# Kernel tuning notes

Measured on AMD Instinct MI355X. Metric: run time of the kernel, lower is better.

## Reference

```python
import jax, jax.numpy as jnp
import numpy as np

E, H, I, T = 8, 1024, 4096, 8192  # experts, hidden, intermediate, total tokens


def setup_inputs() -> dict:
    key = jax.random.key(0)
    k1, k2, k3 = jax.random.split(key, 3)
    hiddens = jax.random.normal(k1, (T, H), dtype=jnp.float32)
    # expert weights, scaled like standard init
    w1_weight = jax.random.normal(k2, (E, H, I), dtype=jnp.float32) * (1.0 / np.sqrt(H).astype(np.float32))
    w2_weight = jax.random.normal(k3, (E, I, H), dtype=jnp.float32) * (1.0 / np.sqrt(I).astype(np.float32))
    # tokens are pre-grouped by expert; equal load of T//E tokens per expert
    batch_sizes = jnp.full((E,), T // E, dtype=jnp.int32)
    return {"hiddens": hiddens, "batch_sizes": batch_sizes,
            "w1_weight": w1_weight, "w2_weight": w2_weight}


def _gmm(x, w, batch_sizes):
    """Grouped matmul: rows of x are grouped contiguously by expert.
    x: [T, K], w: [E, K, N], batch_sizes: [E] (sums to T). Returns [T, N].
    Loop is over the small fixed expert count; each iteration is a dense
    GEMM with rows outside the expert's segment masked to zero.
    """
    n_experts = w.shape[0]
    ends = jnp.cumsum(batch_sizes)
    starts = ends - batch_sizes
    tok = jnp.arange(x.shape[0])[:, None]  # [T, 1]
    out = jnp.zeros((x.shape[0], w.shape[2]), dtype=x.dtype)
    for e in range(n_experts):
        mask = (tok >= starts[e]) & (tok < ends[e])  # [T, 1]
        out = out + jnp.where(mask, x, jnp.zeros((), x.dtype)) @ w[e]
    return out


def reference(hiddens, batch_sizes, w1_weight, w2_weight):
    up = _gmm(hiddens, w1_weight, batch_sizes)    # [T, I]
    down = _gmm(up, w2_weight, batch_sizes)       # [T, H]
    return down
```

## Files before the change

kernel.cpp:

```cpp
#include <hip/hip_runtime.h>
#include <hip/hip_bf16.h>


typedef unsigned short u16;
typedef unsigned int u32;
typedef __attribute__((ext_vector_type(8))) short bf16x8;
typedef __attribute__((ext_vector_type(4))) float f32x4;
typedef __attribute__((ext_vector_type(4))) u32 u32x4;

#define E_N 8
#define H_N 1024
#define I_N 4096
#define T_N 8192

#define GLD2LDS16(g, l)                                                        \
  __builtin_amdgcn_global_load_lds(                                            \
      (const __attribute__((address_space(1))) void*)(g),                      \
      (__attribute__((address_space(3))) void*)(l), 16, 0, 0)

__device__ __forceinline__ u32 pkbf(float lo, float hi) {
  u32 a = __float_as_uint(lo) + 0x8000u;
  u32 b = __float_as_uint(hi) + 0x8000u;
  return __builtin_amdgcn_perm(b, a, 0x07060302u);
}

__device__ __forceinline__ u16 f2bf(float f) {
  __hip_bfloat16 h = __float2bfloat16(f);
  return *(reinterpret_cast<u16*>(&h));
}

__device__ __forceinline__ f32x4 ntload4(const float* p) {
  return __builtin_nontemporal_load((const f32x4*)p);
}

__device__ __forceinline__ int xcd_swz(int bid, int nwg) {
  const int chunk = nwg >> 3;
  return (bid & 7) * chunk + (bid >> 3);
}

#define NB_W1 16384
#define NB_X 4096
#define NB_TR 8192

__global__ __launch_bounds__(256) void prepass_kernel(
    const float* __restrict__ w1, const float* __restrict__ x,
    const float* __restrict__ w2, u16* __restrict__ w1b,
    u16* __restrict__ xb, u16* __restrict__ w2t) {
  __shared__ float tile[64 * 65];
  const int tid = threadIdx.x;
  const int bid = blockIdx.x;

  if (bid < NB_W1 + NB_X) {
    const float* src;
    u16* dst;
    size_t base;
    if (bid < NB_W1) {
      src = w1; dst = w1b; base = (size_t)bid * 2048;
    } else {
      src = x; dst = xb; base = (size_t)(bid - NB_W1) * 2048;
    }
    const size_t i = base + (size_t)tid * 8;
    f32x4 a = ntload4(src + i);
    f32x4 b = ntload4(src + i + 4);
    *(u32x4*)(dst + i) = (u32x4){pkbf(a.x, a.y), pkbf(a.z, a.w),
                                 pkbf(b.x, b.y), pkbf(b.z, b.w)};
    return;
  }

  const int b = bid - (NB_W1 + NB_X);
  const int e = b >> 10;
  const int rem = b & 1023;
  const int i0 = (rem >> 4) * 64;
  const int h0 = (rem & 15) * 64;
  const float* src = w2 + (size_t)e * I_N * H_N;
  u16* dst = w2t + (size_t)e * H_N * I_N;

  {
    const int r = tid >> 4;
    const int c4 = (tid & 15) * 4;
#pragma unroll
    for (int rr = 0; rr < 4; rr++) {
      const int row = rr * 16 + r;
      f32x4 v = ntload4(src + (size_t)(i0 + row) * H_N + h0 + c4);
      tile[row * 65 + c4 + 0] = v.x;
      tile[row * 65 + c4 + 1] = v.y;
      tile[row * 65 + c4 + 2] = v.z;
      tile[row * 65 + c4 + 3] = v.w;
    }
  }
  __syncthreads();

  {
    const int hr = tid >> 3;
    const int ic = (tid & 7) * 8;
#pragma unroll
    for (int hh = 0; hh < 2; hh++) {
      const int h = hh * 32 + hr;
      u32 p[4];
#pragma unroll
      for (int j = 0; j < 4; j++)
        p[j] = pkbf(tile[(ic + 2 * j) * 65 + h], tile[(ic + 2 * j + 1) * 65 + h]);
      *(u32x4*)(dst + (size_t)(h0 + h) * I_N + i0 + ic) =
          (u32x4){p[0], p[1], p[2], p[3]};
    }
  }
}

__global__ __launch_bounds__(256) void wgemm_kernel(const u16* __restrict__ w2t,
                                                    const u16* __restrict__ w1b,
                                                    u16* __restrict__ mt) {
  __shared__ u16 ldsA[4096];
  __shared__ u16 ldsB[4096];

  const int tid = threadIdx.x;
  const int lane = tid & 63;
  const int wv = tid >> 6;
  const int wm = wv >> 1, wn = wv & 1;
  const int lm = lane & 15, quad = lane >> 4;

  const int sbid = xcd_swz(blockIdx.x, 512);
  const int e = sbid >> 6;
  const int t = sbid & 63;
  const int row0 = (t >> 3) * 128;
  const int col0 = (t & 7) * 128;

  const u16* Ae = w2t + (size_t)e * H_N * I_N;
  const u16* Be = w1b + (size_t)e * H_N * I_N;
  u16* mte = mt + (size_t)e * H_N * H_N;

  const int s_r = tid >> 2;
  const int s_k = (tid & 3) * 8;
  const u16* gA0 = Ae + (size_t)(row0 + s_r) * I_N + s_k;
  const u16* gA1 = gA0 + (size_t)64 * I_N;
  const u16* gB0 = Be + (size_t)(col0 + s_r) * I_N + s_k;
  const u16* gB1 = gB0 + (size_t)64 * I_N;
  u16* ldsA_dst = ldsA + wv * 512;
  u16* ldsB_dst = ldsB + wv * 512;

  f32x4 acc[4][4];
#pragma unroll
  for (int i = 0; i < 4; i++)
#pragma unroll
    for (int j = 0; j < 4; j++) acc[i][j] = (f32x4){0.f, 0.f, 0.f, 0.f};

  for (int k0 = 0; k0 < I_N; k0 += 32) {
    GLD2LDS16(gA0 + k0, ldsA_dst);
    GLD2LDS16(gA1 + k0, ldsA_dst + 2048);
    GLD2LDS16(gB0 + k0, ldsB_dst);
    GLD2LDS16(gB1 + k0, ldsB_dst + 2048);

    __syncthreads();

    bf16x8 af[4], bfr[4];
#pragma unroll
    for (int mi = 0; mi < 4; mi++)
      af[mi] = *(const bf16x8*)(ldsA + (wm * 64 + mi * 16 + lm) * 32 + quad * 8);
#pragma unroll
    for (int ni = 0; ni < 4; ni++)
      bfr[ni] = *(const bf16x8*)(ldsB + (wn * 64 + ni * 16 + lm) * 32 + quad * 8);
#pragma unroll
    for (int mi = 0; mi < 4; mi++)
#pragma unroll
      for (int ni = 0; ni < 4; ni++)
        acc[mi][ni] = __builtin_amdgcn_mfma_f32_16x16x32_bf16(
            af[mi], bfr[ni], acc[mi][ni], 0, 0, 0);

    __syncthreads();
  }

  const int orow = row0 + wm * 64 + quad * 4;
  const int ocol = col0 + wn * 64 + lm;
#pragma unroll
  for (int mi = 0; mi < 4; mi++)
#pragma unroll
    for (int ni = 0; ni < 4; ni++)
#pragma unroll
      for (int r = 0; r < 4; r++)
        mte[(size_t)(orow + mi * 16 + r) * H_N + ocol + ni * 16] =
            f2bf(acc[mi][ni][r]);
}

__global__ __launch_bounds__(512, 2) void wgemm8_kernel(
    const u16* __restrict__ w2t, const u16* __restrict__ w1b,
    float* __restrict__ mtp) {
  __shared__ u16 lds[65536];

  const int tid = threadIdx.x;
  const int lane = tid & 63;
  const int wv = tid >> 6;
  const int wm = wv >> 2;
  const int wn = wv & 3;
  const int lm = lane & 15, quad = lane >> 4;

  const int sbid = xcd_swz(blockIdx.x, 256);
  const int kh = sbid >> 7;
  const int rem = sbid & 127;
  const int e = rem >> 4;
  const int t = rem & 15;
  const int row0 = (t >> 2) * 256;
  const int col0 = (t & 3) * 256;

  const u16* Ae = w2t + (size_t)e * H_N * I_N;
  const u16* Be = w1b + (size_t)e * H_N * I_N;

  const int srow = tid >> 3;
  const int koff = ((tid & 7) ^ (srow & 7)) * 8;
  const u16* gA = Ae + (size_t)(row0 + srow) * I_N + koff;
  const u16* gB = Be + (size_t)(col0 + srow) * I_N + koff;
  u16* stA = lds + wv * 512;
  u16* stB = stA + 16384;

  const int sw = (lm & 7) << 4;
  const int c0 = (((quad << 4)) ^ sw) >> 1;
  const int c1 = ((64 | (quad << 4)) ^ sw) >> 1;
  const int rdA = (wm * 128 + lm) * 64;
  const int rdB = (wn * 64 + lm) * 64;

  f32x4 acc[8][4];
#pragma unroll
  for (int i = 0; i < 8; i++)
#pragma unroll
    for (int j = 0; j < 4; j++) acc[i][j] = (f32x4){0.f, 0.f, 0.f, 0.f};

  const int kbeg = kh * (I_N / 2);
  const int NT = (I_N / 2) / 64;

#define STAGE8(bsel, k0)                                                       \
  do {                                                                         \
    u16* la = stA + (bsel)*32768;                                              \
    u16* lb = stB + (bsel)*32768;                                              \
    const u16* ga = gA + (k0);                                                 \
    const u16* gb = gB + (k0);                                                 \
    GLD2LDS16(ga, la);                                                         \
    GLD2LDS16(ga + (size_t)64 * I_N, la + 4096);                               \
    GLD2LDS16(ga + (size_t)128 * I_N, la + 8192);                              \
    GLD2LDS16(ga + (size_t)192 * I_N, la + 12288);                             \
    GLD2LDS16(gb, lb);                                                         \
    GLD2LDS16(gb + (size_t)64 * I_N, lb + 4096);                               \
    GLD2LDS16(gb + (size_t)128 * I_N, lb + 8192);                              \
    GLD2LDS16(gb + (size_t)192 * I_N, lb + 12288);                             \
  } while (0)

  STAGE8(0, kbeg);
  for (int kt = 0; kt < NT; ++kt) {
    if (kt + 1 < NT) {
      STAGE8((kt + 1) & 1, kbeg + (kt + 1) * 64);
      asm volatile("s_waitcnt vmcnt(8)" ::: "memory");
    } else {
      asm volatile("s_waitcnt vmcnt(0)" ::: "memory");
    }
    asm volatile("s_barrier" ::: "memory");

    const u16* bufA = lds + (kt & 1) * 32768;
    const u16* bufB = bufA + 16384;
#pragma unroll
    for (int kh2 = 0; kh2 < 2; ++kh2) {
      const int cc = kh2 ? c1 : c0;
      bf16x8 a[8], b[4];
#pragma unroll
      for (int ni = 0; ni < 4; ni++)
        b[ni] = *(const bf16x8*)(bufB + rdB + ni * 1024 + cc);
#pragma unroll
      for (int mi = 0; mi < 8; mi++)
        a[mi] = *(const bf16x8*)(bufA + rdA + mi * 1024 + cc);
      __builtin_amdgcn_s_setprio(1);
#pragma unroll
      for (int mi = 0; mi < 8; mi++)
#pragma unroll
        for (int ni = 0; ni < 4; ni++)
          acc[mi][ni] = __builtin_amdgcn_mfma_f32_16x16x32_bf16(
              a[mi], b[ni], acc[mi][ni], 0, 0, 0);
      __builtin_amdgcn_s_setprio(0);
    }
    asm volatile("s_barrier" ::: "memory");
  }
#undef STAGE8

  float* dst = mtp + (size_t)(kh * E_N + e) * H_N * H_N;
  const int orow = row0 + wm * 128 + quad * 4;
  const int ocol = col0 + wn * 64 + lm;
#pragma unroll
  for (int mi = 0; mi < 8; mi++)
#pragma unroll
    for (int ni = 0; ni < 4; ni++)
#pragma unroll
      for (int r = 0; r < 4; r++)
        __builtin_nontemporal_store(
            acc[mi][ni][r],
            dst + (size_t)(orow + mi * 16 + r) * H_N + ocol + ni * 16);
}

template <int KSPLIT>
__global__ __launch_bounds__(256) void reduce_mt_kernel(
    const float* __restrict__ mtp, u16* __restrict__ mt) {
  const size_t i = ((size_t)blockIdx.x * 256 + threadIdx.x) * 8;
  float s[8];
#pragma unroll
  for (int j = 0; j < 8; j++) s[j] = 0.f;
#pragma unroll
  for (int p = 0; p < KSPLIT; p++) {
    const float* q = mtp + (size_t)p * E_N * H_N * H_N + i;
    f32x4 a = ntload4(q);
    f32x4 b = ntload4(q + 4);
    s[0] += a.x; s[1] += a.y; s[2] += a.z; s[3] += a.w;
    s[4] += b.x; s[5] += b.y; s[6] += b.z; s[7] += b.w;
  }
  *(u32x4*)(mt + i) = (u32x4){pkbf(s[0], s[1]), pkbf(s[2], s[3]),
                              pkbf(s[4], s[5]), pkbf(s[6], s[7])};
}

__global__ __launch_bounds__(256) void tgemm_kernel(const u16* __restrict__ xb,
                                                    const int* __restrict__ bsz,
                                                    const u16* __restrict__ mt,
                                                    float* __restrict__ out) {
  __shared__ u16 ldsA[2048];
  __shared__ u16 ldsB[4096];

  const int tid = threadIdx.x;
  const int lane = tid & 63;
  const int wv = tid >> 6;
  const int wm = wv >> 1, wn = wv & 1;
  const int lm = lane & 15, quad = lane >> 4;

  const int sbid = xcd_swz(blockIdx.x, 1024);
  const int bm = sbid >> 3, bn = sbid & 7;
  const int row0 = bm * 64;
  const int col0 = bn * 128;

  int e = 0, start = 0;
#pragma unroll
  for (int i = 0; i < E_N; i++) {
    int b = bsz[i];
    if (row0 >= start + b) { start += b; e = i + 1; }
  }
  const u16* mte = mt + (size_t)e * H_N * H_N;

  const int s_r = tid >> 2;
  const int s_k = (tid & 3) * 8;
  const u16* gA0 = xb + (size_t)(row0 + s_r) * H_N + s_k;
  const u16* gB0 = mte + (size_t)(col0 + s_r) * H_N + s_k;
  const u16* gB1 = gB0 + (size_t)64 * H_N;
  u16* ldsA_dst = ldsA + wv * 512;
  u16* ldsB_dst = ldsB + wv * 512;

  f32x4 acc[2][4];
#pragma unroll
  for (int i = 0; i < 2; i++)
#pragma unroll
    for (int j = 0; j < 4; j++) acc[i][j] = (f32x4){0.f, 0.f, 0.f, 0.f};

  for (int k0 = 0; k0 < H_N; k0 += 32) {
    GLD2LDS16(gA0 + k0, ldsA_dst);
    GLD2LDS16(gB0 + k0, ldsB_dst);
    GLD2LDS16(gB1 + k0, ldsB_dst + 2048);

    __syncthreads();

    bf16x8 af[2], bfr[4];
#pragma unroll
    for (int mi = 0; mi < 2; mi++)
      af[mi] = *(const bf16x8*)(ldsA + (wm * 32 + mi * 16 + lm) * 32 + quad * 8);
#pragma unroll
    for (int ni = 0; ni < 4; ni++)
      bfr[ni] = *(const bf16x8*)(ldsB + (wn * 64 + ni * 16 + lm) * 32 + quad * 8);
#pragma unroll
    for (int mi = 0; mi < 2; mi++)
#pragma unroll
      for (int ni = 0; ni < 4; ni++)
        acc[mi][ni] = __builtin_amdgcn_mfma_f32_16x16x32_bf16(
            af[mi], bfr[ni], acc[mi][ni], 0, 0, 0);

    __syncthreads();
  }

  const int orow = row0 + wm * 32 + quad * 4;
  const int ocol = col0 + wn * 64 + lm;
#pragma unroll
  for (int mi = 0; mi < 2; mi++)
#pragma unroll
    for (int ni = 0; ni < 4; ni++)
#pragma unroll
      for (int r = 0; r < 4; r++)
        __builtin_nontemporal_store(
            acc[mi][ni][r],
            out + (size_t)(orow + mi * 16 + r) * H_N + ocol + ni * 16);
}

extern "C" void kernel_launch(void* const* d_in, const int* in_sizes, int n_in,
                              void* d_out, int out_size, void* d_ws,
                              size_t ws_size, hipStream_t stream) {
  (void)in_sizes; (void)n_in; (void)out_size;
  const float* hiddens = (const float*)d_in[0];
  const int* bsz = (const int*)d_in[1];
  const float* w1 = (const float*)d_in[2];
  const float* w2 = (const float*)d_in[3];
  float* out = (float*)d_out;

  char* ws = (char*)d_ws;
  u16* w1b = (u16*)(ws);
  u16* w2t = (u16*)(ws + (size_t)64 * 1024 * 1024);
  u16* xb  = (u16*)(ws + (size_t)128 * 1024 * 1024);
  u16* mt  = (u16*)(ws + (size_t)144 * 1024 * 1024);
  float* mtp = (float*)(ws + (size_t)160 * 1024 * 1024);
  const size_t MiB = 1024 * 1024;

  prepass_kernel<<<dim3(NB_W1 + NB_X + NB_TR), 256, 0, stream>>>(
      w1, hiddens, w2, w1b, xb, w2t);

  if (ws_size >= 224 * MiB) {
    wgemm8_kernel<<<dim3(256), 512, 0, stream>>>(w2t, w1b, mtp);
    reduce_mt_kernel<2><<<dim3(4096), 256, 0, stream>>>(mtp, mt);
  } else {
    wgemm_kernel<<<dim3(512), 256, 0, stream>>>(w2t, w1b, mt);
  }

  tgemm_kernel<<<dim3(1024), 256, 0, stream>>>(xb, bsz, mt, out);
}
```

Before: 410.1 us.

## Rewrite token GEMM with larger tiles, double-buffered LDS and swizzled loads

Replaces the final token-by-fused-weight GEMM with a 512-thread kernel that computes 128x256 tiles, moving from 1024 blocks to 256. K-steps grow to 64 and the LDS stages are double-buffered, so the next tile's loads overlap the current MFMAs. LDS rows use an XOR swizzle to cut bank conflicts, and MFMA issue priority is raised. The larger tile gives more reuse per load, but at 256 blocks occupancy and load balance across CUs may suffer.

```diff
diff --git a/kernel.cpp b/kernel.cpp
--- a/kernel.cpp
+++ b/kernel.cpp
@@ -309,23 +309,23 @@
                               pkbf(s[4], s[5]), pkbf(s[6], s[7])};
 }
 
-__global__ __launch_bounds__(256) void tgemm_kernel(const u16* __restrict__ xb,
-                                                    const int* __restrict__ bsz,
-                                                    const u16* __restrict__ mt,
-                                                    float* __restrict__ out) {
-  __shared__ u16 ldsA[2048];
-  __shared__ u16 ldsB[4096];
+__global__ __launch_bounds__(512, 2) void tgemm8_kernel(
+    const u16* __restrict__ xb, const int* __restrict__ bsz,
+    const u16* __restrict__ mt, float* __restrict__ out) {
+  __shared__ u16 lds[49152];
 
   const int tid = threadIdx.x;
   const int lane = tid & 63;
   const int wv = tid >> 6;
-  const int wm = wv >> 1, wn = wv & 1;
+  const int wm = wv >> 2;
+  const int wn = wv & 3;
   const int lm = lane & 15, quad = lane >> 4;
 
-  const int sbid = xcd_swz(blockIdx.x, 1024);
-  const int bm = sbid >> 3, bn = sbid & 7;
-  const int row0 = bm * 64;
-  const int col0 = bn * 128;
+  const int sbid = xcd_swz(blockIdx.x, 256);
+  const int bm = sbid >> 2;
+  const int bn = sbid & 3;
+  const int row0 = bm * 128;
+  const int col0 = bn * 256;
 
   int e = 0, start = 0;
 #pragma unroll
@@ -335,48 +335,80 @@
   }
   const u16* mte = mt + (size_t)e * H_N * H_N;
 
-  const int s_r = tid >> 2;
-  const int s_k = (tid & 3) * 8;
-  const u16* gA0 = xb + (size_t)(row0 + s_r) * H_N + s_k;
-  const u16* gB0 = mte + (size_t)(col0 + s_r) * H_N + s_k;
-  const u16* gB1 = gB0 + (size_t)64 * H_N;
-  u16* ldsA_dst = ldsA + wv * 512;
-  u16* ldsB_dst = ldsB + wv * 512;
-
-  f32x4 acc[2][4];
-#pragma unroll
-  for (int i = 0; i < 2; i++)
+  const int srow = tid >> 3;
+  const int koff = ((tid & 7) ^ (srow & 7)) * 8;
+  const u16* gA = xb + (size_t)(row0 + srow) * H_N + koff;
+  const u16* gB = mte + (size_t)(col0 + srow) * H_N + koff;
+  u16* stA = lds + wv * 512;
+  u16* stB = stA + 8192;
+
+  const int sw = (lm & 7) << 4;
+  const int c0 = (((quad << 4)) ^ sw) >> 1;
+  const int c1 = ((64 | (quad << 4)) ^ sw) >> 1;
+  const int rdA = (wm * 64 + lm) * 64;
+  const int rdB = (wn * 64 + lm) * 64;
+
+  f32x4 acc[4][4];
+#pragma unroll
+  for (int i = 0; i < 4; i++)
 #pragma unroll
     for (int j = 0; j < 4; j++) acc[i][j] = (f32x4){0.f, 0.f, 0.f, 0.f};
 
-  for (int k0 = 0; k0 < H_N; k0 += 32) {
-    GLD2LDS16(gA0 + k0, ldsA_dst);
-    GLD2LDS16(gB0 + k0, ldsB_dst);
-    GLD2LDS16(gB1 + k0, ldsB_dst + 2048);
-
-    __syncthreads();
-
-    bf16x8 af[2], bfr[4];
-#pragma unroll
-    for (int mi = 0; mi < 2; mi++)
-      af[mi] = *(const bf16x8*)(ldsA + (wm * 32 + mi * 16 + lm) * 32 + quad * 8);
-#pragma unroll
-    for (int ni = 0; ni < 4; ni++)
-      bfr[ni] = *(const bf16x8*)(ldsB + (wn * 64 + ni * 16 + lm) * 32 + quad * 8);
-#pragma unroll
-    for (int mi = 0; mi < 2; mi++)
+  const int NT = H_N / 64;
+
+#define TSTAGE6(bsel, k0)                                                      \
+  do {                                                                         \
+    u16* la = stA + (bsel)*24576;                                              \
+    u16* lb = stB + (bsel)*24576;                                              \
+    const u16* ga = gA + (k0);                                                 \
+    const u16* gb = gB + (k0);                                                 \
+    GLD2LDS16(ga, la);                                                         \
+    GLD2LDS16(ga + (size_t)64 * H_N, la + 4096);                               \
+    GLD2LDS16(gb, lb);                                                         \
+    GLD2LDS16(gb + (size_t)64 * H_N, lb + 4096);                               \
+    GLD2LDS16(gb + (size_t)128 * H_N, lb + 8192);                              \
+    GLD2LDS16(gb + (size_t)192 * H_N, lb + 12288);                             \
+  } while (0)
+
+  TSTAGE6(0, 0);
+  for (int kt = 0; kt < NT; ++kt) {
+    if (kt + 1 < NT) {
+      TSTAGE6((kt + 1) & 1, (kt + 1) * 64);
+      asm volatile("s_waitcnt vmcnt(6)" ::: "memory");
+    } else {
+      asm volatile("s_waitcnt vmcnt(0)" ::: "memory");
+    }
+    asm volatile("s_barrier" ::: "memory");
+
+    const u16* bufA = lds + (kt & 1) * 24576;
+    const u16* bufB = bufA + 8192;
+#pragma unroll
+    for (int kh2 = 0; kh2 < 2; ++kh2) {
+      const int cc = kh2 ? c1 : c0;
+      bf16x8 a[4], b[4];
 #pragma unroll
       for (int ni = 0; ni < 4; ni++)
-        acc[mi][ni] = __builtin_amdgcn_mfma_f32_16x16x32_bf16(
-            af[mi], bfr[ni], acc[mi][ni], 0, 0, 0);
-
-    __syncthreads();
-  }
-
-  const int orow = row0 + wm * 32 + quad * 4;
+        b[ni] = *(const bf16x8*)(bufB + rdB + ni * 1024 + cc);
+#pragma unroll
+      for (int mi = 0; mi < 4; mi++)
+        a[mi] = *(const bf16x8*)(bufA + rdA + mi * 1024 + cc);
+      __builtin_amdgcn_s_setprio(1);
+#pragma unroll
+      for (int mi = 0; mi < 4; mi++)
+#pragma unroll
+        for (int ni = 0; ni < 4; ni++)
+          acc[mi][ni] = __builtin_amdgcn_mfma_f32_16x16x32_bf16(
+              a[mi], b[ni], acc[mi][ni], 0, 0, 0);
+      __builtin_amdgcn_s_setprio(0);
+    }
+    asm volatile("s_barrier" ::: "memory");
+  }
+#undef TSTAGE6
+
+  const int orow = row0 + wm * 64 + quad * 4;
   const int ocol = col0 + wn * 64 + lm;
 #pragma unroll
-  for (int mi = 0; mi < 2; mi++)
+  for (int mi = 0; mi < 4; mi++)
 #pragma unroll
     for (int ni = 0; ni < 4; ni++)
 #pragma unroll
@@ -414,5 +446,5 @@
     wgemm_kernel<<<dim3(512), 256, 0, stream>>>(w2t, w1b, mt);
   }
 
-  tgemm_kernel<<<dim3(1024), 256, 0, stream>>>(xb, bsz, mt, out);
-}
+  tgemm8_kernel<<<dim3(256), 512, 0, stream>>>(xb, bsz, mt, out);
+}
```

Measured after the change: 404.6 us. About the same (-1.3%).
